# Performance work log

Measured on AMD Instinct MI355X. Metric: run time of the kernel, lower is better.

## Reference

```python
import jax, jax.numpy as jnp
import numpy as np
from jax import lax

WIN_SIZE = 11
SIGMA = 1.5
K1, K2 = 0.01, 0.03
DATA_RANGE = 1.0


def _gaussian_window():
    coords = jnp.arange(WIN_SIZE, dtype=jnp.float32) - (WIN_SIZE - 1) / 2.0
    g = jnp.exp(-(coords ** 2) / (2.0 * SIGMA ** 2))
    return g / jnp.sum(g)


def _gaussian_filter(x, win):
    # x: (B, C, H, W); separable depthwise gaussian blur, VALID padding
    C = x.shape[1]
    dn = ('NCHW', 'OIHW', 'NCHW')
    kh = jnp.broadcast_to(win.reshape(1, 1, WIN_SIZE, 1), (C, 1, WIN_SIZE, 1))
    kw = jnp.broadcast_to(win.reshape(1, 1, 1, WIN_SIZE), (C, 1, 1, WIN_SIZE))
    x = lax.conv_general_dilated(x, kh, (1, 1), 'VALID', dimension_numbers=dn, feature_group_count=C)
    x = lax.conv_general_dilated(x, kw, (1, 1), 'VALID', dimension_numbers=dn, feature_group_count=C)
    return x


def _ssim_per_image(X, Y):
    # X, Y: (B, C, H, W) -> (B,) SSIM averaged over channels and spatial (pytorch_msssim, size_average=False)
    win = _gaussian_window()
    C1 = (K1 * DATA_RANGE) ** 2
    C2 = (K2 * DATA_RANGE) ** 2
    mu1 = _gaussian_filter(X, win)
    mu2 = _gaussian_filter(Y, win)
    mu1_sq = mu1 * mu1
    mu2_sq = mu2 * mu2
    mu1_mu2 = mu1 * mu2
    sigma1_sq = _gaussian_filter(X * X, win) - mu1_sq
    sigma2_sq = _gaussian_filter(Y * Y, win) - mu2_sq
    sigma12 = _gaussian_filter(X * Y, win) - mu1_mu2
    ssim_map = ((2.0 * mu1_mu2 + C1) * (2.0 * sigma12 + C2)) / (
        (mu1_sq + mu2_sq + C1) * (sigma1_sq + sigma2_sq + C2))
    return jnp.mean(ssim_map, axis=(1, 2, 3))


def setup_inputs() -> dict:
    key = jax.random.key(0)
    k1, k2 = jax.random.split(key)
    x1 = jax.random.normal(k1, (15, 441, 64), dtype=jnp.float32)
    x2 = jax.random.normal(k2, (5, 5, 441, 64), dtype=jnp.float32)
    return {"x1": x1, "x2": x2}


def reference(x1, x2):
    B, h, w, C = 15, 21, 21, 64
    N, S = x2.shape[0], x2.shape[1]
    # queries: view(15,21,21,64).permute(0,3,1,2) -> (15,64,21,21)
    q = jnp.transpose(x1.reshape(B, h, w, C), (0, 3, 1, 2))
    # per-(h,w) L2 normalization over channel dim (dim 0 of each sample)
    q = q / jnp.linalg.norm(q, axis=1, keepdims=True)
    # supports: (N,5,441,64).permute(0,1,3,2).view -> (N,5,64,21,21)
    s = jnp.transpose(x2, (0, 1, 3, 2)).reshape(N, S, C, h, w)
    s = s / jnp.linalg.norm(s, axis=2, keepdims=True)
    # pairwise broadcast: every query against every support image of every class
    Xb = jnp.broadcast_to(q[:, None, None], (B, N, S, C, h, w)).reshape(B * N * S, C, h, w)
    Yb = jnp.broadcast_to(s[None], (B, N, S, C, h, w)).reshape(B * N * S, C, h, w)
    sims = _ssim_per_image(Xb, Yb).reshape(B, N, S)
    # inner_sim[0, j] = sum of SSIM over the S shots
    return jnp.sum(sims, axis=2)  # (15, N)
```

## Files before the change

kernel.cpp:

```cpp
#include <hip/hip_runtime.h>

#define BQ   15
#define NIMG 40
#define CH   64
#define HW   21
#define P    441
#define WIN  11
#define OH   11
#define OP   121
#define TP   231

__device__ __forceinline__ float Wf(int a) {
    constexpr float w[WIN] = {
        0.0010283804f, 0.0075988025f, 0.0360007770f, 0.1093606993f,
        0.2130055427f, 0.2660117290f, 0.2130055427f, 0.1093606993f,
        0.0360007770f, 0.0075988025f, 0.0010283804f};
    return w[a];
}

__global__ void __launch_bounds__(256) prep_kernel(const float* __restrict__ x1,
                                                   const float* __restrict__ x2,
                                                   float* __restrict__ tn) {
    int img = blockIdx.x;
    int p0  = blockIdx.y * 63;
    const float* src = (img < BQ) ? (x1 + (size_t)img * P * CH)
                                  : (x2 + (size_t)(img - BQ) * P * CH);
    float* dst = tn + (size_t)img * CH * P;

    __shared__ float tile[63 * 65];
    __shared__ float invn[63];

    for (int i = threadIdx.x; i < 63 * CH; i += 256) {
        int p = i >> 6, c = i & 63;
        tile[p * 65 + c] = src[(size_t)p0 * CH + i];
    }
    __syncthreads();
    if (threadIdx.x < 63) {
        int p = threadIdx.x;
        float s = 0.f;
#pragma unroll
        for (int c = 0; c < CH; ++c) { float v = tile[p * 65 + c]; s += v * v; }
        invn[p] = rsqrtf(s);
    }
    __syncthreads();
    for (int i = threadIdx.x; i < 63 * CH; i += 256) {
        int c = i / 63, p = i - c * 63;
        dst[(size_t)c * P + p0 + p] = tile[p * 65 + c] * invn[p];
    }
}

__global__ void __launch_bounds__(256) stats_kernel(const float* __restrict__ tn,
                                                    float* __restrict__ mu,
                                                    float* __restrict__ sq) {
    __shared__ float lds[8 * 920];
    int cb = blockIdx.x * 8;

    for (int i = threadIdx.x; i < 8 * P; i += 256) {
        int k = i / P, t = i - k * P;
        lds[k * 920 + t] = tn[(size_t)(cb + k) * P + t];
    }
    __syncthreads();
    for (int i = threadIdx.x; i < 8 * TP; i += 256) {
        int k = i / TP, t = i - k * TP;
        const float* x = lds + k * 920;
        float a1 = 0.f, a2 = 0.f;
#pragma unroll
        for (int a = 0; a < WIN; ++a) {
            float v = x[t + 21 * a];
            a1 = fmaf(Wf(a), v, a1);
            a2 = fmaf(Wf(a) * v, v, a2);
        }
        lds[k * 920 + 448 + t] = a1;
        lds[k * 920 + 684 + t] = a2;
    }
    __syncthreads();
    for (int i = threadIdx.x; i < 8 * OP; i += 256) {
        int k = i / OP, t = i - k * OP;
        int r = t / OH, cc = t - r * OH;
        int b0 = r * HW + cc;
        const float* t1 = lds + k * 920 + 448;
        const float* t2 = lds + k * 920 + 684;
        float a1 = 0.f, a2 = 0.f;
#pragma unroll
        for (int a = 0; a < WIN; ++a) {
            a1 = fmaf(Wf(a), t1[b0 + a], a1);
            a2 = fmaf(Wf(a), t2[b0 + a], a2);
        }
        size_t o = (size_t)(cb + k) * OP + t;
        mu[o] = a1;
        sq[o] = a2;
    }
}

__global__ void __launch_bounds__(256) pairs_kernel(const float* __restrict__ tn,
                                                    const float* __restrict__ mu,
                                                    const float* __restrict__ sq,
                                                    float* __restrict__ out) {
    __shared__ float lds[16 * 684];
    __shared__ float ws4[4];

    int pair = blockIdx.x;
    int b    = pair / 25;
    int rem  = pair - b * 25;
    int cb   = blockIdx.y * 16;

    const float* X = tn + ((size_t)b * CH + cb) * P;
    const float* Y = tn + ((size_t)(BQ + rem) * CH + cb) * P;

    for (int i = threadIdx.x; i < 16 * P; i += 256) {
        int k = i / P, t = i - k * P;
        lds[k * 684 + t] = X[(size_t)k * P + t] * Y[(size_t)k * P + t];
    }
    __syncthreads();
    for (int i = threadIdx.x; i < 16 * TP; i += 256) {
        int k = i / TP, t = i - k * TP;
        const float* x = lds + k * 684;
        float a1 = 0.f;
#pragma unroll
        for (int a = 0; a < WIN; ++a) a1 = fmaf(Wf(a), x[t + 21 * a], a1);
        lds[k * 684 + 448 + t] = a1;
    }
    __syncthreads();

    const float C1 = 1e-4f, C2 = 9e-4f;
    size_t oq = ((size_t)b * CH + cb) * OP;
    size_t os = ((size_t)(BQ + rem) * CH + cb) * OP;
    float part = 0.f;
    for (int i = threadIdx.x; i < 16 * OP; i += 256) {
        int k = i / OP, t = i - k * OP;
        int r = t / OH, cc = t - r * OH;
        const float* t1 = lds + k * 684 + 448;
        float sxy = 0.f;
#pragma unroll
        for (int a = 0; a < WIN; ++a) sxy = fmaf(Wf(a), t1[r * HW + cc + a], sxy);
        float m1 = mu[oq + k * OP + t], m2 = mu[os + k * OP + t];
        float v1 = sq[oq + k * OP + t] - m1 * m1;
        float v2 = sq[os + k * OP + t] - m2 * m2;
        float cov = sxy - m1 * m2;
        part += ((2.f * m1 * m2 + C1) * (2.f * cov + C2)) /
                ((m1 * m1 + m2 * m2 + C1) * (v1 + v2 + C2));
    }

#pragma unroll
    for (int off = 32; off > 0; off >>= 1) part += __shfl_down(part, off, 64);
    if ((threadIdx.x & 63) == 0) ws4[threadIdx.x >> 6] = part;
    __syncthreads();
    if (threadIdx.x == 0) {
        int n = rem / 5;
        atomicAdd(&out[b * 5 + n],
                  (ws4[0] + ws4[1] + ws4[2] + ws4[3]) * (1.0f / (CH * OP)));
    }
}

extern "C" void kernel_launch(void* const* d_in, const int* in_sizes, int n_in,
                              void* d_out, int out_size, void* d_ws, size_t ws_size,
                              hipStream_t stream) {
    const float* x1 = (const float*)d_in[0];
    const float* x2 = (const float*)d_in[1];
    float* out = (float*)d_out;
    float* ws  = (float*)d_ws;

    float* tn = ws;
    float* mu = tn + (size_t)NIMG * CH * P;
    float* sq = mu + (size_t)NIMG * CH * OP;

    hipMemsetAsync(d_out, 0, (size_t)out_size * sizeof(float), stream);

    prep_kernel<<<dim3(NIMG, 7), 256, 0, stream>>>(x1, x2, tn);
    stats_kernel<<<NIMG * CH / 8, 256, 0, stream>>>(tn, mu, sq);
    pairs_kernel<<<dim3(375, 4), 256, 0, stream>>>(tn, mu, sq, out);
}
```

Measured before the change: 100.8 us.

## Compute separable blur in registers with wave shuffles instead of LDS passes

```diff
diff --git a/kernel.cpp b/kernel.cpp
--- a/kernel.cpp
+++ b/kernel.cpp
@@ -8,7 +8,6 @@
 #define WIN  11
 #define OH   11
 #define OP   121
-#define TP   231
 
 __device__ __forceinline__ float Wf(int a) {
     constexpr float w[WIN] = {
@@ -20,7 +19,11 @@
 
 __global__ void __launch_bounds__(256) prep_kernel(const float* __restrict__ x1,
                                                    const float* __restrict__ x2,
-                                                   float* __restrict__ tn) {
+                                                   float* __restrict__ tn,
+                                                   float* __restrict__ out) {
+    if (blockIdx.x == 0 && blockIdx.y == 0 && threadIdx.x < BQ * 5)
+        out[threadIdx.x] = 0.f;
+
     int img = blockIdx.x;
     int p0  = blockIdx.y * 63;
     const float* src = (img < BQ) ? (x1 + (size_t)img * P * CH)
@@ -52,43 +55,47 @@
 __global__ void __launch_bounds__(256) stats_kernel(const float* __restrict__ tn,
                                                     float* __restrict__ mu,
                                                     float* __restrict__ sq) {
-    __shared__ float lds[8 * 920];
-    int cb = blockIdx.x * 8;
+    int lane = threadIdx.x & 63, w = threadIdx.x >> 6;
+    int k = lane / HW, j = lane - k * HW;
+    int ic = blockIdx.x * 12 + w * 3 + k;
+    bool vch = (k < 3) && (ic < NIMG * CH);
+    const float* X = tn + (size_t)(vch ? ic : 0) * P;
 
-    for (int i = threadIdx.x; i < 8 * P; i += 256) {
-        int k = i / P, t = i - k * P;
-        lds[k * 920 + t] = tn[(size_t)(cb + k) * P + t];
+    float t1[OH], t2[OH];
+#pragma unroll
+    for (int r = 0; r < OH; ++r) { t1[r] = 0.f; t2[r] = 0.f; }
+#pragma unroll
+    for (int i = 0; i < HW; ++i) {
+        float x = vch ? X[i * HW + j] : 0.f;
+        float xx = x * x;
+#pragma unroll
+        for (int r = 0; r < OH; ++r) {
+            int a = i - r;
+            if (a >= 0 && a < WIN) {
+                t1[r] = fmaf(Wf(a), x, t1[r]);
+                t2[r] = fmaf(Wf(a), xx, t2[r]);
+            }
+        }
     }
-    __syncthreads();
-    for (int i = threadIdx.x; i < 8 * TP; i += 256) {
-        int k = i / TP, t = i - k * TP;
-        const float* x = lds + k * 920;
-        float a1 = 0.f, a2 = 0.f;
+    float o1[OH], o2[OH];
 #pragma unroll
-        for (int a = 0; a < WIN; ++a) {
-            float v = x[t + 21 * a];
-            a1 = fmaf(Wf(a), v, a1);
-            a2 = fmaf(Wf(a) * v, v, a2);
+    for (int r = 0; r < OH; ++r) {
+        float a1 = Wf(0) * t1[r];
+        float a2 = Wf(0) * t2[r];
+#pragma unroll
+        for (int a = 1; a < WIN; ++a) {
+            a1 = fmaf(Wf(a), __shfl(t1[r], lane + a), a1);
+            a2 = fmaf(Wf(a), __shfl(t2[r], lane + a), a2);
         }
-        lds[k * 920 + 448 + t] = a1;
-        lds[k * 920 + 684 + t] = a2;
+        o1[r] = a1; o2[r] = a2;
     }
-    __syncthreads();
-    for (int i = threadIdx.x; i < 8 * OP; i += 256) {
-        int k = i / OP, t = i - k * OP;
-        int r = t / OH, cc = t - r * OH;
-        int b0 = r * HW + cc;
-        const float* t1 = lds + k * 920 + 448;
-        const float* t2 = lds + k * 920 + 684;
-        float a1 = 0.f, a2 = 0.f;
+    if (vch && j < OH) {
+        size_t o = (size_t)ic * OP + j;
 #pragma unroll
-        for (int a = 0; a < WIN; ++a) {
-            a1 = fmaf(Wf(a), t1[b0 + a], a1);
-            a2 = fmaf(Wf(a), t2[b0 + a], a2);
+        for (int r = 0; r < OH; ++r) {
+            mu[o + r * OH] = o1[r];
+            sq[o + r * OH] = o2[r];
         }
-        size_t o = (size_t)(cb + k) * OP + t;
-        mu[o] = a1;
-        sq[o] = a2;
     }
 }
 
@@ -96,54 +103,60 @@
                                                     const float* __restrict__ mu,
                                                     const float* __restrict__ sq,
                                                     float* __restrict__ out) {
-    __shared__ float lds[16 * 684];
-    __shared__ float ws4[4];
-
     int pair = blockIdx.x;
     int b    = pair / 25;
     int rem  = pair - b * 25;
-    int cb   = blockIdx.y * 16;
+    int lane = threadIdx.x & 63, w = threadIdx.x >> 6;
+    int k = lane / HW, j = lane - k * HW;
+    int c = blockIdx.y * 12 + w * 3 + k;
+    bool vch = (k < 3) && (c < CH);
+    int cs = vch ? c : 0;
 
-    const float* X = tn + ((size_t)b * CH + cb) * P;
-    const float* Y = tn + ((size_t)(BQ + rem) * CH + cb) * P;
+    const float* X = tn + ((size_t)b * CH + cs) * P;
+    const float* Y = tn + ((size_t)(BQ + rem) * CH + cs) * P;
 
-    for (int i = threadIdx.x; i < 16 * P; i += 256) {
-        int k = i / P, t = i - k * P;
-        lds[k * 684 + t] = X[(size_t)k * P + t] * Y[(size_t)k * P + t];
+    float t1[OH];
+#pragma unroll
+    for (int r = 0; r < OH; ++r) t1[r] = 0.f;
+#pragma unroll
+    for (int i = 0; i < HW; ++i) {
+        float xy = vch ? X[i * HW + j] * Y[i * HW + j] : 0.f;
+#pragma unroll
+        for (int r = 0; r < OH; ++r) {
+            int a = i - r;
+            if (a >= 0 && a < WIN) t1[r] = fmaf(Wf(a), xy, t1[r]);
+        }
     }
-    __syncthreads();
-    for (int i = threadIdx.x; i < 16 * TP; i += 256) {
-        int k = i / TP, t = i - k * TP;
-        const float* x = lds + k * 684;
-        float a1 = 0.f;
+    float o[OH];
 #pragma unroll
-        for (int a = 0; a < WIN; ++a) a1 = fmaf(Wf(a), x[t + 21 * a], a1);
-        lds[k * 684 + 448 + t] = a1;
+    for (int r = 0; r < OH; ++r) {
+        float a1 = Wf(0) * t1[r];
+#pragma unroll
+        for (int a = 1; a < WIN; ++a)
+            a1 = fmaf(Wf(a), __shfl(t1[r], lane + a), a1);
+        o[r] = a1;
     }
-    __syncthreads();
 
     const float C1 = 1e-4f, C2 = 9e-4f;
-    size_t oq = ((size_t)b * CH + cb) * OP;
-    size_t os = ((size_t)(BQ + rem) * CH + cb) * OP;
     float part = 0.f;
-    for (int i = threadIdx.x; i < 16 * OP; i += 256) {
-        int k = i / OP, t = i - k * OP;
-        int r = t / OH, cc = t - r * OH;
-        const float* t1 = lds + k * 684 + 448;
-        float sxy = 0.f;
+    if (vch && j < OH) {
+        size_t oq = ((size_t)b * CH + c) * OP + j;
+        size_t os = ((size_t)(BQ + rem) * CH + c) * OP + j;
 #pragma unroll
-        for (int a = 0; a < WIN; ++a) sxy = fmaf(Wf(a), t1[r * HW + cc + a], sxy);
-        float m1 = mu[oq + k * OP + t], m2 = mu[os + k * OP + t];
-        float v1 = sq[oq + k * OP + t] - m1 * m1;
-        float v2 = sq[os + k * OP + t] - m2 * m2;
-        float cov = sxy - m1 * m2;
-        part += ((2.f * m1 * m2 + C1) * (2.f * cov + C2)) /
-                ((m1 * m1 + m2 * m2 + C1) * (v1 + v2 + C2));
+        for (int r = 0; r < OH; ++r) {
+            float m1 = mu[oq + r * OH], m2 = mu[os + r * OH];
+            float v1 = sq[oq + r * OH] - m1 * m1;
+            float v2 = sq[os + r * OH] - m2 * m2;
+            float cov = o[r] - m1 * m2;
+            part += ((2.f * m1 * m2 + C1) * (2.f * cov + C2)) /
+                    ((m1 * m1 + m2 * m2 + C1) * (v1 + v2 + C2));
+        }
     }
 
 #pragma unroll
     for (int off = 32; off > 0; off >>= 1) part += __shfl_down(part, off, 64);
-    if ((threadIdx.x & 63) == 0) ws4[threadIdx.x >> 6] = part;
+    __shared__ float ws4[4];
+    if ((threadIdx.x & 63) == 0) ws4[w] = part;
     __syncthreads();
     if (threadIdx.x == 0) {
         int n = rem / 5;
@@ -164,9 +177,7 @@
     float* mu = tn + (size_t)NIMG * CH * P;
     float* sq = mu + (size_t)NIMG * CH * OP;
 
-    hipMemsetAsync(d_out, 0, (size_t)out_size * sizeof(float), stream);
-
-    prep_kernel<<<dim3(NIMG, 7), 256, 0, stream>>>(x1, x2, tn);
-    stats_kernel<<<NIMG * CH / 8, 256, 0, stream>>>(tn, mu, sq);
-    pairs_kernel<<<dim3(375, 4), 256, 0, stream>>>(tn, mu, sq, out);
+    prep_kernel<<<dim3(NIMG, 7), 256, 0, stream>>>(x1, x2, tn, out);
+    stats_kernel<<<(NIMG * CH + 11) / 12, 256, 0, stream>>>(tn, mu, sq);
+    pairs_kernel<<<dim3(375, 6), 256, 0, stream>>>(tn, mu, sq, out);
 }
```

Result: slower. 105.0 us (+4.2%).
